# Kernel tuning notes

Measured on AMD Instinct MI355X. Metric: run time of the kernel, lower is better.

Reference implementation:

```python
import jax, jax.numpy as jnp
import numpy as np
import math

B, T, E, H, QL, SUB = 4, 2048, 64, 8, 6, 64  # batch, win_len, n_embd, n_head, q_len, sub_len


def _row_mask(index, sub_len, win_len):
    log_l = math.ceil(np.log2(sub_len))
    mask = np.zeros(win_len, dtype=np.float32)
    if (win_len // sub_len) * 2 * log_l > index:
        mask[: index + 1] = 1
    else:
        while index >= 0:
            if index - log_l + 1 < 0:
                mask[:index] = 1
                break
            mask[index - log_l + 1 : index + 1] = 1
            for i in range(log_l):
                new_index = index - log_l + 1 - 2 ** i
                if index - new_index <= sub_len and new_index >= 0:
                    mask[new_index] = 1
            index -= sub_len
    return mask


def _log_mask(win_len, sub_len):
    m = np.zeros((win_len, win_len), dtype=np.float32)
    for i in range(win_len):
        m[i] = _row_mask(i, sub_len, win_len)
    return m.reshape(1, 1, win_len, win_len)


def setup_inputs() -> dict:
    key = jax.random.key(0)
    ks = jax.random.split(key, 4)
    x = jax.random.normal(ks[0], (B, T, E), dtype=jnp.float32)
    Wqk = jax.random.normal(ks[1], (2 * H * E, E, QL), dtype=jnp.float32) * 0.02
    bqk = jnp.zeros((2 * H * E,), dtype=jnp.float32)
    Wv = jax.random.normal(ks[2], (E, H * E), dtype=jnp.float32) * 0.02
    bv = jnp.zeros((H * E,), dtype=jnp.float32)
    Wp = jax.random.normal(ks[3], (H * E, E), dtype=jnp.float32) * 0.02
    bp = jnp.zeros((E,), dtype=jnp.float32)
    mask = jnp.asarray(_log_mask(T, SUB).astype(bool))  # [1,1,T,T] bool
    return {"x": x, "Wqk": Wqk, "bqk": bqk, "Wv": Wv, "bv": bv,
            "Wp": Wp, "bp": bp, "mask": mask}


def reference(x, Wqk, bqk, Wv, bv, Wp, bp, mask):
    b, t, e = x.shape
    h = Wv.shape[1] // e
    ql = Wqk.shape[-1]

    # value projection (Conv1D rf=1 == dense)
    value = x @ Wv + bv                              # [B,T,H*E]

    # causal conv1d QK projection: left-pad by q_len-1
    xc = jnp.transpose(x, (0, 2, 1))                 # [B,E,T]
    qk = jax.lax.conv_general_dilated(
        xc, Wqk, window_strides=(1,), padding=[(ql - 1, 0)],
        dimension_numbers=("NCH", "OIH", "NCH"))    # [B,2*H*E,T]
    qk = qk + bqk[None, :, None]
    qk = jnp.transpose(qk, (0, 2, 1))                # [B,T,2*H*E]
    query, key_ = jnp.split(qk, 2, axis=2)

    q = query.reshape(b, t, h, e).transpose(0, 2, 1, 3)   # [B,H,T,E]
    k = key_.reshape(b, t, h, e).transpose(0, 2, 3, 1)    # [B,H,E,T]
    v = value.reshape(b, t, h, e).transpose(0, 2, 1, 3)   # [B,H,T,E]

    pre = jnp.einsum("bhqe,bhek->bhqk", q, k) / jnp.sqrt(jnp.asarray(e, x.dtype))
    m = mask[:, :, :t, :t].astype(pre.dtype)
    pre = pre * m + (-1e9) * (1.0 - m)
    attn_weights = jax.nn.softmax(pre, axis=-1)           # [B,H,T,T]
    # dropout p=0.0 -> identity
    attn = jnp.einsum("bhqk,bhke->bhqe", attn_weights, v)  # [B,H,T,E]
    attn = attn.transpose(0, 2, 1, 3).reshape(b, t, h * e)
    out = attn @ Wp + bp                                  # [B,T,E]
    return out, attn_weights
```

## Files before the change

kernel.cpp:

```cpp
#include <hip/hip_runtime.h>
#include <hip/hip_bf16.h>


typedef __attribute__((ext_vector_type(8))) short bf16x8;
typedef __attribute__((ext_vector_type(4))) float f32x4;
typedef unsigned int uint32;

#define MFMA16(a, b, c) __builtin_amdgcn_mfma_f32_16x16x32_bf16((a), (b), (c), 0, 0, 0)

static __device__ __forceinline__ bool sparse_pred(int r, int c) {
  int d = r - c;
  if (d < 0) return false;
  int o = d & 63;
  int j = c + o;
  bool inS = (o <= 7) || (o == 9) || (o == 13) || (o == 21) || (o == 37);
  return (j >= 5) ? inS : (o >= 1);
}

static __device__ __forceinline__ uint32 bfbits(float x) {
  __hip_bfloat16 h = __float2bfloat16(x);
  unsigned short u;
  __builtin_memcpy(&u, &h, 2);
  return (uint32)u;
}

static __device__ __forceinline__ unsigned pred4(bool causal, int ct, int rt, int q, int nt,
                                                 int lq, const unsigned* pm4) {
  const int tb = ct * 64 + 16 * nt + 4 * lq;
  const int thr = q - tb;
  const unsigned cb = (thr < 0) ? 0u : (thr >= 3 ? 0xFu : (0xFu >> (3 - thr)));
  if (causal) return (ct < rt) ? 0xFu : cb;
  if (ct == 0) {
    unsigned p = 0;
#pragma unroll
    for (int reg = 0; reg < 4; ++reg) p |= (unsigned)sparse_pred(q, tb + reg) << reg;
    return p;
  }
  unsigned p = pm4[nt];
  if (ct == rt) p &= cb;
  return p;
}

__global__ void prep_kernel(const float* __restrict__ Wqk, const float* __restrict__ Wv,
                            __hip_bfloat16* __restrict__ Wt_qk, __hip_bfloat16* __restrict__ Wv_t) {
  int idx = blockIdx.x * 256 + threadIdx.x;
  if (idx < 1024 * 384) {
    int o = idx / 384, kidx = idx - o * 384;
    int kk = kidx >> 6, i = kidx & 63;
    Wt_qk[idx] = __float2bfloat16(Wqk[(o * 64 + i) * 6 + kk]);
  } else {
    int j = idx - 1024 * 384;
    int n = j >> 6, k = j & 63;
    Wv_t[j] = __float2bfloat16(Wv[k * 512 + n]);
  }
}

__global__ __launch_bounds__(256, 4) void proj_kernel(
    const float* __restrict__ x, const float* __restrict__ bqk, const float* __restrict__ bv,
    const __hip_bfloat16* __restrict__ Wt_qk, const __hip_bfloat16* __restrict__ Wv_t,
    __hip_bfloat16* __restrict__ q_bf, __hip_bfloat16* __restrict__ k_bf,
    __hip_bfloat16* __restrict__ v_bf) {
  const int tokTile = blockIdx.x;
  const int chTile = blockIdx.y;
  const int gt0 = tokTile * 64;
  const int b = gt0 >> 11;
  const int t0 = gt0 & 2047;
  const int thr = threadIdx.x;
  __shared__ __align__(16) __hip_bfloat16 xwin[69][72];
  __shared__ __align__(16) __hip_bfloat16 vt[64][72];

  for (int u = thr; u < 69 * 64; u += 256) {
    int row = u >> 6, i = u & 63;
    int t = t0 - 5 + row;
    float v = (t >= 0) ? x[((size_t)b * 2048 + t) * 64 + i] : 0.f;
    xwin[row][i] = __float2bfloat16(v);
  }
  __syncthreads();

  const int wave = thr >> 6, lane = thr & 63;
  const int lm = lane & 15, lq = lane >> 4;
  f32x4 acc[4];
#pragma unroll
  for (int nb = 0; nb < 4; ++nb) acc[nb] = (f32x4){0.f, 0.f, 0.f, 0.f};

  if (chTile < 16) {
    const int ch0 = chTile * 64;
    for (int kc = 0; kc < 12; ++kc) {
      int k0 = kc * 32 + lq * 8;
      int kk = k0 >> 6, i0 = k0 & 63;
      bf16x8 a = *reinterpret_cast<const bf16x8*>(&xwin[16 * wave + lm + kk][i0]);
#pragma unroll
      for (int nb = 0; nb < 4; ++nb) {
        bf16x8 bb =
            *reinterpret_cast<const bf16x8*>(&Wt_qk[(size_t)(ch0 + 16 * nb + lm) * 384 + k0]);
        acc[nb] = MFMA16(a, bb, acc[nb]);
      }
    }
#pragma unroll
    for (int nb = 0; nb < 4; ++nb) {
      int e = 16 * nb + lm;
      float bias = bqk[chTile * 64 + e];
#pragma unroll
      for (int reg = 0; reg < 4; ++reg)
        vt[16 * wave + lq * 4 + reg][e] = __float2bfloat16(acc[nb][reg] + bias);
    }
    __syncthreads();
    const int half = (chTile >> 3) & 1;
    const int h = chTile & 7;
    __hip_bfloat16* dst = half ? k_bf : q_bf;
    for (int u = thr; u < 512; u += 256) {
      int row = u >> 3, c8 = u & 7;
      *reinterpret_cast<uint4*>(dst + ((size_t)((b * 8 + h) * 2048 + t0 + row)) * 64 + c8 * 8) =
          *reinterpret_cast<const uint4*>(&vt[row][c8 * 8]);
    }
  } else {
    const int nv0 = (chTile - 16) * 64;
    for (int kc = 0; kc < 2; ++kc) {
      int i0 = kc * 32 + lq * 8;
      bf16x8 a = *reinterpret_cast<const bf16x8*>(&xwin[16 * wave + lm + 5][i0]);
#pragma unroll
      for (int nb = 0; nb < 4; ++nb) {
        bf16x8 bb = *reinterpret_cast<const bf16x8*>(&Wv_t[(size_t)(nv0 + 16 * nb + lm) * 64 + i0]);
        acc[nb] = MFMA16(a, bb, acc[nb]);
      }
    }
#pragma unroll
    for (int nb = 0; nb < 4; ++nb) {
      int e = 16 * nb + lm;
      float bias = bv[nv0 + e];
#pragma unroll
      for (int reg = 0; reg < 4; ++reg)
        vt[e][16 * wave + lq * 4 + reg] = __float2bfloat16(acc[nb][reg] + bias);
    }
    __syncthreads();
    const int h = chTile - 16;
    for (int u = thr; u < 512; u += 256) {
      int e = u >> 3, c8 = u & 7;
      *reinterpret_cast<uint4*>(v_bf + ((size_t)((b * 8 + h) * 64 + e)) * 2048 + t0 + c8 * 8) =
          *reinterpret_cast<const uint4*>(&vt[e][c8 * 8]);
    }
  }
}

__global__ __launch_bounds__(256, 2) void attn_kernel(
    const __hip_bfloat16* __restrict__ q_bf, const __hip_bfloat16* __restrict__ k_bf,
    const __hip_bfloat16* __restrict__ v_bf,
    float* __restrict__ attn, float* __restrict__ attnout) {
  const int linear = (int)blockIdx.y * 16 + (int)blockIdx.x;
  const int xcd = linear & 7;
  const int slot = linear >> 3;
  const int bh = xcd * 4 + (slot >> 4);
  const int tb = slot & 15;
  const int tid = threadIdx.x;
  const int wave = tid >> 6;
  const int lane = tid & 63;
  const int lm = lane & 15, lq = lane >> 4;

  __shared__ __align__(16) __hip_bfloat16 kbuf[2][4096];
  __shared__ __align__(16) __hip_bfloat16 vbuf[2][4096];
  __shared__ __align__(16) __hip_bfloat16 psw[4][16 * 72];
  __hip_bfloat16* pw = psw[wave];

  const int b2 = bh >> 3, h = bh & 7;
  const char* kbhB = (const char*)(k_bf + (size_t)bh * 2048 * 64);
  const char* vbhB = (const char*)(v_bf + (size_t)bh * 64 * 2048);

  int Ls[2], sK[2], sV[2];
#pragma unroll
  for (int i = 0; i < 2; ++i) {
    const int L = i * 4096 + tid * 16;
    const int r = L >> 7, c = L & 127;
    const int cs = c ^ ((r & 7) << 4);
    Ls[i] = L;
    sK[i] = r * 128 + cs;
    sV[i] = r * 4096 + cs;
  }
  const int fx = (lm & 7) << 4;
  const int fc0 = (lq * 16) ^ fx;
  const int fc1 = (64 + lq * 16) ^ fx;

  const int q64 = 16 * wave + lm;
  unsigned pm4[4];
  {
    const int S[12] = {0, 1, 2, 3, 4, 5, 6, 7, 9, 13, 21, 37};
    unsigned long long M = 0;
#pragma unroll
    for (int i = 0; i < 12; ++i) M |= 1ull << ((q64 - S[i]) & 63);
#pragma unroll
    for (int nt = 0; nt < 4; ++nt) pm4[nt] = (unsigned)((M >> (16 * nt + 4 * lq)) & 0xFull);
  }

  for (int task = 0; task < 2; ++task) {
    const int rt = (task == 0) ? tb : 31 - tb;
    const int r0 = rt * 64;
    const bool causal = (rt < 6);
    const int q = r0 + q64;

    const __hip_bfloat16* qrow = q_bf + ((size_t)bh * 2048 + q) * 64;
    bf16x8 qa0 = *reinterpret_cast<const bf16x8*>(qrow + lq * 8);
    bf16x8 qa1 = *reinterpret_cast<const bf16x8*>(qrow + 32 + lq * 8);

    uint4 ks0, ks1, vs0, vs1;

    {
      const char* kt = kbhB;
      ks0 = *reinterpret_cast<const uint4*>(kt + sK[0]);
      ks1 = *reinterpret_cast<const uint4*>(kt + sK[1]);
      *reinterpret_cast<uint4*>((char*)kbuf[0] + Ls[0]) = ks0;
      *reinterpret_cast<uint4*>((char*)kbuf[0] + Ls[1]) = ks1;
    }
    __syncthreads();
    float lsum = 0.f;
    for (int ct = 0; ct <= rt; ++ct) {
      if (ct < rt) {
        const char* kt = kbhB + (size_t)(ct + 1) * 8192;
        ks0 = *reinterpret_cast<const uint4*>(kt + sK[0]);
        ks1 = *reinterpret_cast<const uint4*>(kt + sK[1]);
      }
      const char* kb = (const char*)kbuf[ct & 1];
#pragma unroll
      for (int nt = 0; nt < 4; ++nt) {
        const int rb = (16 * nt + lm) * 128;
        bf16x8 ka0 = *reinterpret_cast<const bf16x8*>(kb + rb + fc0);
        bf16x8 ka1 = *reinterpret_cast<const bf16x8*>(kb + rb + fc1);
        f32x4 c = (f32x4){0.f, 0.f, 0.f, 0.f};
        c = MFMA16(ka0, qa0, c);
        c = MFMA16(ka1, qa1, c);
        const unsigned p = pred4(causal, ct, rt, q, nt, lq, pm4);
#pragma unroll
        for (int reg = 0; reg < 4; ++reg)
          lsum += ((p >> reg) & 1u) ? __expf(c[reg] * 0.125f) : 0.f;
      }
      if (ct < rt) {
        char* kw = (char*)kbuf[(ct + 1) & 1];
        *reinterpret_cast<uint4*>(kw + Ls[0]) = ks0;
        *reinterpret_cast<uint4*>(kw + Ls[1]) = ks1;
      }
      __syncthreads();
    }
    lsum += __shfl_xor(lsum, 16);
    lsum += __shfl_xor(lsum, 32);
    const float inv = 1.f / lsum;

    f32x4 oacc[4];
#pragma unroll
    for (int eb = 0; eb < 4; ++eb) oacc[eb] = (f32x4){0.f, 0.f, 0.f, 0.f};
    float* aq = attn + ((size_t)bh * 2048 + q) * 2048;

    {
      const char* kt = kbhB;
      ks0 = *reinterpret_cast<const uint4*>(kt + sK[0]);
      ks1 = *reinterpret_cast<const uint4*>(kt + sK[1]);
      const char* vt = vbhB;
      vs0 = *reinterpret_cast<const uint4*>(vt + sV[0]);
      vs1 = *reinterpret_cast<const uint4*>(vt + sV[1]);
      *reinterpret_cast<uint4*>((char*)kbuf[0] + Ls[0]) = ks0;
      *reinterpret_cast<uint4*>((char*)kbuf[0] + Ls[1]) = ks1;
      *reinterpret_cast<uint4*>((char*)vbuf[0] + Ls[0]) = vs0;
      *reinterpret_cast<uint4*>((char*)vbuf[0] + Ls[1]) = vs1;
    }
    __syncthreads();
    for (int ct = 0; ct <= rt; ++ct) {
      if (ct < rt) {
        const char* kt = kbhB + (size_t)(ct + 1) * 8192;
        ks0 = *reinterpret_cast<const uint4*>(kt + sK[0]);
        ks1 = *reinterpret_cast<const uint4*>(kt + sK[1]);
        const char* vt = vbhB + (size_t)(ct + 1) * 128;
        vs0 = *reinterpret_cast<const uint4*>(vt + sV[0]);
        vs1 = *reinterpret_cast<const uint4*>(vt + sV[1]);
      }
      const char* kb = (const char*)kbuf[ct & 1];
      const char* vb = (const char*)vbuf[ct & 1];
#pragma unroll
      for (int nt = 0; nt < 4; ++nt) {
        const int rb = (16 * nt + lm) * 128;
        bf16x8 ka0 = *reinterpret_cast<const bf16x8*>(kb + rb + fc0);
        bf16x8 ka1 = *reinterpret_cast<const bf16x8*>(kb + rb + fc1);
        f32x4 c = (f32x4){0.f, 0.f, 0.f, 0.f};
        c = MFMA16(ka0, qa0, c);
        c = MFMA16(ka1, qa1, c);
        const unsigned p = pred4(causal, ct, rt, q, nt, lq, pm4);
        f32x4 w;
#pragma unroll
        for (int reg = 0; reg < 4; ++reg)
          w[reg] = ((p >> reg) & 1u) ? __expf(c[reg] * 0.125f) * inv : 0.f;
        __builtin_nontemporal_store(w, reinterpret_cast<f32x4*>(aq + ct * 64 + 16 * nt + 4 * lq));
        uint32 u0 = bfbits(w[0]) | (bfbits(w[1]) << 16);
        uint32 u1 = bfbits(w[2]) | (bfbits(w[3]) << 16);
        uint2 uu = {u0, u1};
        *reinterpret_cast<uint2*>(&pw[lm * 72 + 16 * nt + 4 * lq]) = uu;
      }
      bf16x8 pa0 = *reinterpret_cast<const bf16x8*>(&pw[lm * 72 + lq * 8]);
      bf16x8 pa1 = *reinterpret_cast<const bf16x8*>(&pw[lm * 72 + 32 + lq * 8]);
#pragma unroll
      for (int eb = 0; eb < 4; ++eb) {
        const int rb = (16 * eb + lm) * 128;
        bf16x8 va0 = *reinterpret_cast<const bf16x8*>(vb + rb + fc0);
        bf16x8 va1 = *reinterpret_cast<const bf16x8*>(vb + rb + fc1);
        oacc[eb] = MFMA16(va0, pa0, oacc[eb]);
        oacc[eb] = MFMA16(va1, pa1, oacc[eb]);
      }
      if (ct < rt) {
        char* kw = (char*)kbuf[(ct + 1) & 1];
        *reinterpret_cast<uint4*>(kw + Ls[0]) = ks0;
        *reinterpret_cast<uint4*>(kw + Ls[1]) = ks1;
        char* vw = (char*)vbuf[(ct + 1) & 1];
        *reinterpret_cast<uint4*>(vw + Ls[0]) = vs0;
        *reinterpret_cast<uint4*>(vw + Ls[1]) = vs1;
      }
      __syncthreads();
    }

    float* oq = attnout + ((size_t)(b2 * 2048 + q)) * 512 + h * 64;
#pragma unroll
    for (int eb = 0; eb < 4; ++eb)
      *reinterpret_cast<f32x4*>(oq + 16 * eb + 4 * lq) = oacc[eb];
  }
}

__global__ __launch_bounds__(256, 4) void outproj_kernel(const float* __restrict__ attnout,
                                                         const float* __restrict__ Wp,
                                                         const float* __restrict__ bp,
                                                         float* __restrict__ out) {
  __shared__ __align__(16) float wp_s[128][64];
  const int thr = threadIdx.x;
  const int wave = thr >> 6, lane = thr & 63;
  const int row0 = blockIdx.x * 16 + wave * 4;
  float acc[4] = {0.f, 0.f, 0.f, 0.f};
  for (int kt = 0; kt < 4; ++kt) {
    __syncthreads();
    for (int u = thr; u < 2048; u += 256) {
      int r = u >> 4, c4 = (u & 15) * 4;
      *reinterpret_cast<float4*>(&wp_s[r][c4]) =
          *reinterpret_cast<const float4*>(&Wp[(size_t)(kt * 128 + r) * 64 + c4]);
    }
    __syncthreads();
    for (int k4 = 0; k4 < 32; ++k4) {
      float wv0 = wp_s[k4 * 4 + 0][lane];
      float wv1 = wp_s[k4 * 4 + 1][lane];
      float wv2 = wp_s[k4 * 4 + 2][lane];
      float wv3 = wp_s[k4 * 4 + 3][lane];
#pragma unroll
      for (int rr = 0; rr < 4; ++rr) {
        const float4 a = *reinterpret_cast<const float4*>(
            &attnout[(size_t)(row0 + rr) * 512 + kt * 128 + k4 * 4]);
        acc[rr] += a.x * wv0 + a.y * wv1 + a.z * wv2 + a.w * wv3;
      }
    }
  }
  const float bias = bp[lane];
#pragma unroll
  for (int rr = 0; rr < 4; ++rr) out[(size_t)(row0 + rr) * 64 + lane] = acc[rr] + bias;
}

extern "C" void kernel_launch(void* const* d_in, const int* in_sizes, int n_in, void* d_out,
                              int out_size, void* d_ws, size_t ws_size, hipStream_t stream) {
  (void)in_sizes;
  (void)n_in;
  (void)out_size;
  (void)ws_size;
  const float* x = (const float*)d_in[0];
  const float* Wqk = (const float*)d_in[1];
  const float* bqk = (const float*)d_in[2];
  const float* Wv = (const float*)d_in[3];
  const float* bv = (const float*)d_in[4];
  const float* Wp = (const float*)d_in[5];
  const float* bp = (const float*)d_in[6];

  float* out = (float*)d_out;
  float* attn = out + (size_t)4 * 2048 * 64;

  char* ws = (char*)d_ws;
  __hip_bfloat16* q_bf = (__hip_bfloat16*)(ws);
  __hip_bfloat16* k_bf = (__hip_bfloat16*)(ws + (size_t)8 * 1024 * 1024);
  __hip_bfloat16* v_bf = (__hip_bfloat16*)(ws + (size_t)16 * 1024 * 1024);
  float* attnout = (float*)(ws + (size_t)24 * 1024 * 1024);
  __hip_bfloat16* Wt_qk = (__hip_bfloat16*)(ws + (size_t)40 * 1024 * 1024);
  __hip_bfloat16* Wv_t = (__hip_bfloat16*)(ws + (size_t)41 * 1024 * 1024);

  hipLaunchKernelGGL(prep_kernel, dim3(1664), dim3(256), 0, stream, Wqk, Wv, Wt_qk, Wv_t);
  hipLaunchKernelGGL(proj_kernel, dim3(128, 24), dim3(256), 0, stream, x, bqk, bv, Wt_qk, Wv_t,
                     q_bf, k_bf, v_bf);
  hipLaunchKernelGGL(attn_kernel, dim3(16, 32), dim3(256), 0, stream, q_bf, k_bf, v_bf, attn,
                     attnout);
  hipLaunchKernelGGL(outproj_kernel, dim3(512), dim3(256), 0, stream, attnout, Wp, bp, out);
}
```

Measured before the change: 672.7 us.

## Stage two K/V tiles per barrier and use regular stores for attn

Doubles the shared-memory K/V staging buffers so each loop iteration loads and processes two 64-column tiles, which halves the number of __syncthreads barriers and gives each prefetch more compute to hide behind. It also replaces the nontemporal store of attention weights with a plain store. The larger LDS footprint (about 68KB per block) may limit how many blocks fit per CU under launch_bounds(256,2). The changed store type may alter cache and write behaviour for the large attn output.

```diff
diff --git a/kernel.cpp b/kernel.cpp
--- a/kernel.cpp
+++ b/kernel.cpp
@@ -156,8 +156,8 @@
   const int lane = tid & 63;
   const int lm = lane & 15, lq = lane >> 4;
 
-  __shared__ __align__(16) __hip_bfloat16 kbuf[2][4096];
-  __shared__ __align__(16) __hip_bfloat16 vbuf[2][4096];
+  __shared__ __align__(16) __hip_bfloat16 kbuf[2][8192];
+  __shared__ __align__(16) __hip_bfloat16 vbuf[2][8192];
   __shared__ __align__(16) __hip_bfloat16 psw[4][16 * 72];
   __hip_bfloat16* pw = psw[wave];
 
@@ -165,15 +165,17 @@
   const char* kbhB = (const char*)(k_bf + (size_t)bh * 2048 * 64);
   const char* vbhB = (const char*)(v_bf + (size_t)bh * 64 * 2048);
 
-  int Ls[2], sK[2], sV[2];
-#pragma unroll
-  for (int i = 0; i < 2; ++i) {
+  int Ls[4], sK[4], sV[4];
+#pragma unroll
+  for (int i = 0; i < 4; ++i) {
     const int L = i * 4096 + tid * 16;
-    const int r = L >> 7, c = L & 127;
+    const int t2 = L >> 13;
+    const int r = (L >> 7) & 63;
+    const int c = L & 127;
     const int cs = c ^ ((r & 7) << 4);
     Ls[i] = L;
-    sK[i] = r * 128 + cs;
-    sV[i] = r * 4096 + cs;
+    sK[i] = t2 * 8192 + r * 128 + cs;
+    sV[i] = t2 * 128 + r * 4096 + cs;
   }
   const int fx = (lm & 7) << 4;
   const int fc0 = (lq * 16) ^ fx;
@@ -200,41 +202,44 @@
     bf16x8 qa0 = *reinterpret_cast<const bf16x8*>(qrow + lq * 8);
     bf16x8 qa1 = *reinterpret_cast<const bf16x8*>(qrow + 32 + lq * 8);
 
-    uint4 ks0, ks1, vs0, vs1;
-
-    {
-      const char* kt = kbhB;
-      ks0 = *reinterpret_cast<const uint4*>(kt + sK[0]);
-      ks1 = *reinterpret_cast<const uint4*>(kt + sK[1]);
-      *reinterpret_cast<uint4*>((char*)kbuf[0] + Ls[0]) = ks0;
-      *reinterpret_cast<uint4*>((char*)kbuf[0] + Ls[1]) = ks1;
-    }
+    uint4 kp[4], vp[4];
+
+#pragma unroll
+    for (int i = 0; i < 4; ++i) kp[i] = *reinterpret_cast<const uint4*>(kbhB + sK[i]);
+#pragma unroll
+    for (int i = 0; i < 4; ++i) *reinterpret_cast<uint4*>((char*)kbuf[0] + Ls[i]) = kp[i];
     __syncthreads();
     float lsum = 0.f;
-    for (int ct = 0; ct <= rt; ++ct) {
-      if (ct < rt) {
-        const char* kt = kbhB + (size_t)(ct + 1) * 8192;
-        ks0 = *reinterpret_cast<const uint4*>(kt + sK[0]);
-        ks1 = *reinterpret_cast<const uint4*>(kt + sK[1]);
-      }
-      const char* kb = (const char*)kbuf[ct & 1];
-#pragma unroll
-      for (int nt = 0; nt < 4; ++nt) {
-        const int rb = (16 * nt + lm) * 128;
-        bf16x8 ka0 = *reinterpret_cast<const bf16x8*>(kb + rb + fc0);
-        bf16x8 ka1 = *reinterpret_cast<const bf16x8*>(kb + rb + fc1);
-        f32x4 c = (f32x4){0.f, 0.f, 0.f, 0.f};
-        c = MFMA16(ka0, qa0, c);
-        c = MFMA16(ka1, qa1, c);
-        const unsigned p = pred4(causal, ct, rt, q, nt, lq, pm4);
-#pragma unroll
-        for (int reg = 0; reg < 4; ++reg)
-          lsum += ((p >> reg) & 1u) ? __expf(c[reg] * 0.125f) : 0.f;
-      }
-      if (ct < rt) {
-        char* kw = (char*)kbuf[(ct + 1) & 1];
-        *reinterpret_cast<uint4*>(kw + Ls[0]) = ks0;
-        *reinterpret_cast<uint4*>(kw + Ls[1]) = ks1;
+    for (int ctp = 0; ctp <= rt; ctp += 2) {
+      const bool pf = (ctp + 2 <= rt);
+      if (pf) {
+#pragma unroll
+        for (int i = 0; i < 4; ++i)
+          kp[i] = *reinterpret_cast<const uint4*>(kbhB + (size_t)(ctp + 2) * 8192 + sK[i]);
+      }
+      const char* kb = (const char*)kbuf[(ctp >> 1) & 1];
+#pragma unroll
+      for (int ts = 0; ts < 2; ++ts) {
+        const int ct = ctp + ts;
+        if (ts == 1 && ct > rt) break;
+#pragma unroll
+        for (int nt = 0; nt < 4; ++nt) {
+          const int rb = ts * 8192 + (16 * nt + lm) * 128;
+          bf16x8 ka0 = *reinterpret_cast<const bf16x8*>(kb + rb + fc0);
+          bf16x8 ka1 = *reinterpret_cast<const bf16x8*>(kb + rb + fc1);
+          f32x4 c = (f32x4){0.f, 0.f, 0.f, 0.f};
+          c = MFMA16(ka0, qa0, c);
+          c = MFMA16(ka1, qa1, c);
+          const unsigned p = pred4(causal, ct, rt, q, nt, lq, pm4);
+#pragma unroll
+          for (int reg = 0; reg < 4; ++reg)
+            lsum += ((p >> reg) & 1u) ? __expf(c[reg] * 0.125f) : 0.f;
+        }
+      }
+      if (pf) {
+        char* kw = (char*)kbuf[((ctp >> 1) + 1) & 1];
+#pragma unroll
+        for (int i = 0; i < 4; ++i) *reinterpret_cast<uint4*>(kw + Ls[i]) = kp[i];
       }
       __syncthreads();
     }
@@ -247,66 +252,70 @@
     for (int eb = 0; eb < 4; ++eb) oacc[eb] = (f32x4){0.f, 0.f, 0.f, 0.f};
     float* aq = attn + ((size_t)bh * 2048 + q) * 2048;
 
-    {
-      const char* kt = kbhB;
-      ks0 = *reinterpret_cast<const uint4*>(kt + sK[0]);
-      ks1 = *reinterpret_cast<const uint4*>(kt + sK[1]);
-      const char* vt = vbhB;
-      vs0 = *reinterpret_cast<const uint4*>(vt + sV[0]);
-      vs1 = *reinterpret_cast<const uint4*>(vt + sV[1]);
-      *reinterpret_cast<uint4*>((char*)kbuf[0] + Ls[0]) = ks0;
-      *reinterpret_cast<uint4*>((char*)kbuf[0] + Ls[1]) = ks1;
-      *reinterpret_cast<uint4*>((char*)vbuf[0] + Ls[0]) = vs0;
-      *reinterpret_cast<uint4*>((char*)vbuf[0] + Ls[1]) = vs1;
-    }
-    __syncthreads();
-    for (int ct = 0; ct <= rt; ++ct) {
-      if (ct < rt) {
-        const char* kt = kbhB + (size_t)(ct + 1) * 8192;
-        ks0 = *reinterpret_cast<const uint4*>(kt + sK[0]);
-        ks1 = *reinterpret_cast<const uint4*>(kt + sK[1]);
-        const char* vt = vbhB + (size_t)(ct + 1) * 128;
-        vs0 = *reinterpret_cast<const uint4*>(vt + sV[0]);
-        vs1 = *reinterpret_cast<const uint4*>(vt + sV[1]);
-      }
-      const char* kb = (const char*)kbuf[ct & 1];
-      const char* vb = (const char*)vbuf[ct & 1];
-#pragma unroll
-      for (int nt = 0; nt < 4; ++nt) {
-        const int rb = (16 * nt + lm) * 128;
-        bf16x8 ka0 = *reinterpret_cast<const bf16x8*>(kb + rb + fc0);
-        bf16x8 ka1 = *reinterpret_cast<const bf16x8*>(kb + rb + fc1);
-        f32x4 c = (f32x4){0.f, 0.f, 0.f, 0.f};
-        c = MFMA16(ka0, qa0, c);
-        c = MFMA16(ka1, qa1, c);
-        const unsigned p = pred4(causal, ct, rt, q, nt, lq, pm4);
-        f32x4 w;
-#pragma unroll
-        for (int reg = 0; reg < 4; ++reg)
-          w[reg] = ((p >> reg) & 1u) ? __expf(c[reg] * 0.125f) * inv : 0.f;
-        __builtin_nontemporal_store(w, reinterpret_cast<f32x4*>(aq + ct * 64 + 16 * nt + 4 * lq));
-        uint32 u0 = bfbits(w[0]) | (bfbits(w[1]) << 16);
-        uint32 u1 = bfbits(w[2]) | (bfbits(w[3]) << 16);
-        uint2 uu = {u0, u1};
-        *reinterpret_cast<uint2*>(&pw[lm * 72 + 16 * nt + 4 * lq]) = uu;
-      }
-      bf16x8 pa0 = *reinterpret_cast<const bf16x8*>(&pw[lm * 72 + lq * 8]);
-      bf16x8 pa1 = *reinterpret_cast<const bf16x8*>(&pw[lm * 72 + 32 + lq * 8]);
-#pragma unroll
-      for (int eb = 0; eb < 4; ++eb) {
-        const int rb = (16 * eb + lm) * 128;
-        bf16x8 va0 = *reinterpret_cast<const bf16x8*>(vb + rb + fc0);
-        bf16x8 va1 = *reinterpret_cast<const bf16x8*>(vb + rb + fc1);
-        oacc[eb] = MFMA16(va0, pa0, oacc[eb]);
-        oacc[eb] = MFMA16(va1, pa1, oacc[eb]);
-      }
-      if (ct < rt) {
-        char* kw = (char*)kbuf[(ct + 1) & 1];
-        *reinterpret_cast<uint4*>(kw + Ls[0]) = ks0;
-        *reinterpret_cast<uint4*>(kw + Ls[1]) = ks1;
-        char* vw = (char*)vbuf[(ct + 1) & 1];
-        *reinterpret_cast<uint4*>(vw + Ls[0]) = vs0;
-        *reinterpret_cast<uint4*>(vw + Ls[1]) = vs1;
+#pragma unroll
+    for (int i = 0; i < 4; ++i) {
+      kp[i] = *reinterpret_cast<const uint4*>(kbhB + sK[i]);
+      vp[i] = *reinterpret_cast<const uint4*>(vbhB + sV[i]);
+    }
+#pragma unroll
+    for (int i = 0; i < 4; ++i) {
+      *reinterpret_cast<uint4*>((char*)kbuf[0] + Ls[i]) = kp[i];
+      *reinterpret_cast<uint4*>((char*)vbuf[0] + Ls[i]) = vp[i];
+    }
+    __syncthreads();
+    for (int ctp = 0; ctp <= rt; ctp += 2) {
+      const bool pf = (ctp + 2 <= rt);
+      if (pf) {
+#pragma unroll
+        for (int i = 0; i < 4; ++i) {
+          kp[i] = *reinterpret_cast<const uint4*>(kbhB + (size_t)(ctp + 2) * 8192 + sK[i]);
+          vp[i] = *reinterpret_cast<const uint4*>(vbhB + (size_t)(ctp + 2) * 128 + sV[i]);
+        }
+      }
+      const char* kb = (const char*)kbuf[(ctp >> 1) & 1];
+      const char* vb = (const char*)vbuf[(ctp >> 1) & 1];
+#pragma unroll
+      for (int ts = 0; ts < 2; ++ts) {
+        const int ct = ctp + ts;
+        if (ts == 1 && ct > rt) break;
+#pragma unroll
+        for (int nt = 0; nt < 4; ++nt) {
+          const int rb = ts * 8192 + (16 * nt + lm) * 128;
+          bf16x8 ka0 = *reinterpret_cast<const bf16x8*>(kb + rb + fc0);
+          bf16x8 ka1 = *reinterpret_cast<const bf16x8*>(kb + rb + fc1);
+          f32x4 c = (f32x4){0.f, 0.f, 0.f, 0.f};
+          c = MFMA16(ka0, qa0, c);
+          c = MFMA16(ka1, qa1, c);
+          const unsigned p = pred4(causal, ct, rt, q, nt, lq, pm4);
+          f32x4 w;
+#pragma unroll
+          for (int reg = 0; reg < 4; ++reg)
+            w[reg] = ((p >> reg) & 1u) ? __expf(c[reg] * 0.125f) * inv : 0.f;
+          *reinterpret_cast<f32x4*>(aq + ct * 64 + 16 * nt + 4 * lq) = w;
+          uint32 u0 = bfbits(w[0]) | (bfbits(w[1]) << 16);
+          uint32 u1 = bfbits(w[2]) | (bfbits(w[3]) << 16);
+          uint2 uu = {u0, u1};
+          *reinterpret_cast<uint2*>(&pw[lm * 72 + 16 * nt + 4 * lq]) = uu;
+        }
+        bf16x8 pa0 = *reinterpret_cast<const bf16x8*>(&pw[lm * 72 + lq * 8]);
+        bf16x8 pa1 = *reinterpret_cast<const bf16x8*>(&pw[lm * 72 + 32 + lq * 8]);
+#pragma unroll
+        for (int eb = 0; eb < 4; ++eb) {
+          const int rb = ts * 8192 + (16 * eb + lm) * 128;
+          bf16x8 va0 = *reinterpret_cast<const bf16x8*>(vb + rb + fc0);
+          bf16x8 va1 = *reinterpret_cast<const bf16x8*>(vb + rb + fc1);
+          oacc[eb] = MFMA16(va0, pa0, oacc[eb]);
+          oacc[eb] = MFMA16(va1, pa1, oacc[eb]);
+        }
+      }
+      if (pf) {
+        char* kw = (char*)kbuf[((ctp >> 1) + 1) & 1];
+        char* vw = (char*)vbuf[((ctp >> 1) + 1) & 1];
+#pragma unroll
+        for (int i = 0; i < 4; ++i) {
+          *reinterpret_cast<uint4*>(kw + Ls[i]) = kp[i];
+          *reinterpret_cast<uint4*>(vw + Ls[i]) = vp[i];
+        }
       }
       __syncthreads();
     }
```

Measured after the change: 734.5 us. +9.2%, slower.
